# Kernel optimization log

Measured on AMD Instinct MI355X. Metric: run time of the kernel, lower is better.

## Reference

```python
import jax, jax.numpy as jnp
import numpy as np

B, S, D_MODEL, H, DK, DV, DOUT = 8, 2048, 1024, 1, 512, 512, 1024
EPS = 1e-6
TEMP = DK ** 0.5


def _ln(x, g, b):
    # LayerNorm over last dim, eps=1e-6, affine
    m = jnp.mean(x, axis=-1, keepdims=True)
    v = jnp.mean((x - m) ** 2, axis=-1, keepdims=True)
    return (x - m) * jax.lax.rsqrt(v + EPS) * g + b


def setup_inputs() -> dict:
    key = jax.random.key(0)
    ks = jax.random.split(key, 16)
    s = 0.02
    return {
        "q": jax.random.normal(ks[0], (B, S, D_MODEL), jnp.float32),
        "k": jax.random.normal(ks[1], (B, S, D_MODEL), jnp.float32),
        "v": jax.random.normal(ks[2], (B, S, D_MODEL), jnp.float32),
        "mask": jnp.ones((B, S, S), jnp.int32),
        "Wq": jax.random.normal(ks[3], (D_MODEL, H * DK), jnp.float32) * s,
        "bq": jnp.zeros((H * DK,), jnp.float32),
        "Wk": jax.random.normal(ks[4], (D_MODEL, H * DK), jnp.float32) * s,
        "bk": jnp.zeros((H * DK,), jnp.float32),
        "Wv": jax.random.normal(ks[5], (D_MODEL, H * DV), jnp.float32) * s,
        "bv": jnp.zeros((H * DV,), jnp.float32),
        "g_q": jnp.ones((H * DK,), jnp.float32),
        "be_q": jnp.zeros((H * DK,), jnp.float32),
        "g_k": jnp.ones((H * DK,), jnp.float32),
        "be_k": jnp.zeros((H * DK,), jnp.float32),
        "g_v": jnp.ones((H * DV,), jnp.float32),
        "be_v": jnp.zeros((H * DV,), jnp.float32),
        "W1": jax.random.normal(ks[6], (H * DV, H * DV), jnp.float32) * s,
        "b1": jnp.zeros((H * DV,), jnp.float32),
        "W2": jax.random.normal(ks[7], (H * DV, DOUT), jnp.float32) * s,
        "b2": jnp.zeros((DOUT,), jnp.float32),
    }


def reference(q, k, v, mask, Wq, bq, Wk, bk, Wv, bv, g_q, be_q, g_k, be_k, g_v, be_v, W1, b1, W2, b2):
    # QKV projections, viewed as (B, S, H, d)
    qp = (q @ Wq + bq).reshape(B, S, H, DK)
    kp = (k @ Wk + bk).reshape(B, S, H, DK)
    vp = (v @ Wv + bv).reshape(B, S, H, DV)
    residual = qp
    # per-(token,head) LayerNorm over last dim (valid only because H == 1 in source)
    qn = jnp.swapaxes(_ln(qp, g_q, be_q), 1, 2)  # (B, H, S, DK)
    kn = jnp.swapaxes(_ln(kp, g_k, be_k), 1, 2)
    vn = jnp.swapaxes(_ln(vp, g_v, be_v), 1, 2)
    # scaled dot-product attention with mask
    scores = jnp.einsum('bhqd,bhkd->bhqk', qn / TEMP, kn)
    scores = jnp.where(mask[:, None, :, :] == 0, -1e9, scores)
    attn = jax.nn.softmax(scores, axis=-1)
    out = jnp.einsum('bhqk,bhkd->bhqd', attn, vn)
    out = jnp.swapaxes(out, 1, 2).reshape(B, S, H * DV)
    # trailing 2-layer MLP
    out = jax.nn.relu(out @ W1 + b1) @ W2 + b2
    return (out, residual, jnp.squeeze(attn))
```

## Files before the change

### kernel.cpp

```cpp
#include <hip/hip_runtime.h>
#include <hip/hip_bf16.h>

typedef __attribute__((ext_vector_type(8))) short short8;
typedef __attribute__((ext_vector_type(4))) short short4v;
typedef __attribute__((ext_vector_type(4))) float f32x4;

#define INV_TEMP 0.044194173824159216f

__device__ __forceinline__ ushort f2bf(float f) {
  unsigned u = __float_as_uint(f);
  unsigned r = (u + 0x7FFFu + ((u >> 16) & 1u)) >> 16;
  return (ushort)r;
}
__device__ __forceinline__ float bf2f(ushort u) {
  union { unsigned i; float f; } x; x.i = ((unsigned)u) << 16; return x.f;
}

__device__ __forceinline__ void gload_lds16(const void* g, void* l) {
  __builtin_amdgcn_global_load_lds(
      (const __attribute__((address_space(1))) unsigned int*)(unsigned long long)(uintptr_t)g,
      (__attribute__((address_space(3))) unsigned int*)(unsigned)(uintptr_t)l,
      16, 0, 0);
}

__global__ __launch_bounds__(256)
void transpose_cvt_all(const float* __restrict__ Wq, const float* __restrict__ Wk,
                       const float* __restrict__ Wv, const float* __restrict__ W1,
                       const float* __restrict__ W2,
                       ushort* __restrict__ Tq, ushort* __restrict__ Tk,
                       ushort* __restrict__ Tv, ushort* __restrict__ T1,
                       ushort* __restrict__ T2) {
  const int z = blockIdx.z;
  const int K = (z < 3) ? 1024 : 512;
  const int N = (z == 4) ? 1024 : 512;
  if (blockIdx.x * 32 >= N || blockIdx.y * 32 >= K) return;
  const float* W = z == 0 ? Wq : (z == 1 ? Wk : (z == 2 ? Wv : (z == 3 ? W1 : W2)));
  ushort* WT = z == 0 ? Tq : (z == 1 ? Tk : (z == 2 ? Tv : (z == 3 ? T1 : T2)));
  __shared__ float tile[32][33];
  const int n0 = blockIdx.x * 32, k0 = blockIdx.y * 32;
  const int tx = threadIdx.x & 31, ty = threadIdx.x >> 5;
  #pragma unroll
  for (int i = ty; i < 32; i += 8)
    tile[i][tx] = W[(long)(k0 + i) * N + n0 + tx];
  __syncthreads();
  #pragma unroll
  for (int i = ty; i < 32; i += 8)
    WT[(long)(n0 + i) * K + k0 + tx] = f2bf(tile[tx][i]);
}

__global__ __launch_bounds__(256)
void transpose_bf16(const ushort* __restrict__ in, ushort* __restrict__ out, int S, int D) {
  __shared__ ushort tile[32][33];
  const ushort* inb = in + (long)blockIdx.z * S * D;
  ushort* outb = out + (long)blockIdx.z * S * D;
  const int d0 = blockIdx.x * 32, s0 = blockIdx.y * 32;
  const int tx = threadIdx.x & 31, ty = threadIdx.x >> 5;
  #pragma unroll
  for (int i = ty; i < 32; i += 8)
    tile[i][tx] = inb[(long)(s0 + i) * D + d0 + tx];
  __syncthreads();
  #pragma unroll
  for (int i = ty; i < 32; i += 8)
    outb[(long)(d0 + i) * S + s0 + tx] = tile[tx][i];
}

__global__ __launch_bounds__(256)
void ln3_kernel(const float* __restrict__ Xq, const ushort* __restrict__ Xk,
                const ushort* __restrict__ Xv,
                const float* __restrict__ gq, const float* __restrict__ beq,
                const float* __restrict__ gk, const float* __restrict__ bek,
                const float* __restrict__ gv, const float* __restrict__ bev,
                ushort* __restrict__ Oq, ushort* __restrict__ Ok, ushort* __restrict__ Ov) {
  const int which = blockIdx.y;
  const float* g = which == 0 ? gq : (which == 1 ? gk : gv);
  const float* be = which == 0 ? beq : (which == 1 ? bek : bev);
  ushort* out = which == 0 ? Oq : (which == 1 ? Ok : Ov);
  const float scale = which == 0 ? INV_TEMP : 1.0f;

  const int row = blockIdx.x * 4 + (threadIdx.x >> 6);
  const int lane = threadIdx.x & 63;
  f32x4 v0, v1;
  if (which == 0) {
    const float* x = Xq + (long)row * 512 + lane * 8;
    v0 = *(const f32x4*)x;
    v1 = *(const f32x4*)(x + 4);
  } else {
    const ushort* x = (which == 1 ? Xk : Xv) + (long)row * 512 + lane * 8;
    short8 vv = *(const short8*)x;
    #pragma unroll
    for (int j = 0; j < 4; j++) { v0[j] = bf2f((ushort)vv[j]); v1[j] = bf2f((ushort)vv[4 + j]); }
  }
  float s = v0[0]+v0[1]+v0[2]+v0[3]+v1[0]+v1[1]+v1[2]+v1[3];
  float ss = v0[0]*v0[0]+v0[1]*v0[1]+v0[2]*v0[2]+v0[3]*v0[3]
           + v1[0]*v1[0]+v1[1]*v1[1]+v1[2]*v1[2]+v1[3]*v1[3];
  #pragma unroll
  for (int off = 32; off; off >>= 1) { s += __shfl_xor(s, off); ss += __shfl_xor(ss, off); }
  const float mean = s * (1.0f/512.0f);
  const float var  = ss * (1.0f/512.0f) - mean*mean;
  const float rs = rsqrtf(var + 1e-6f);
  f32x4 g0 = *(const f32x4*)(g + lane*8);
  f32x4 g1 = *(const f32x4*)(g + lane*8 + 4);
  f32x4 b0 = *(const f32x4*)(be + lane*8);
  f32x4 b1 = *(const f32x4*)(be + lane*8 + 4);
  union { short8 v; ushort u[8]; } o;
  #pragma unroll
  for (int j = 0; j < 4; j++) o.u[j]     = f2bf(((v0[j]-mean)*rs*g0[j] + b0[j]) * scale);
  #pragma unroll
  for (int j = 0; j < 4; j++) o.u[4 + j] = f2bf(((v1[j]-mean)*rs*g1[j] + b1[j]) * scale);
  *(short8*)(out + (long)row * 512 + lane * 8) = o.v;
}

template<int EPI, bool HAS_BIAS, bool OUT_BF16, bool A_F32>
__global__ __launch_bounds__(256)
void gemm_tn_pipe(const void* __restrict__ Av, const ushort* __restrict__ Bt,
                  const float* __restrict__ bias, const int* __restrict__ mask,
                  float* __restrict__ Cf, ushort* __restrict__ Cb,
                  float* __restrict__ partial,
                  const float* __restrict__ A2, const float* __restrict__ A3,
                  const ushort* __restrict__ Bt2, const ushort* __restrict__ Bt3,
                  const float* __restrict__ bias2, const float* __restrict__ bias3,
                  ushort* __restrict__ Cb2,
                  int M, int N, int K,
                  long sA, long sB, long sC, long sMask) {
  __shared__ ushort As[2][128 * 64];
  __shared__ ushort Bs[2][128 * 64];
  __shared__ float zloc[128];
  const int tid = threadIdx.x;
  const int lane = tid & 63;
  const int wave = tid >> 6;
  const int wr = wave >> 1;
  const int wc = wave & 1;

  const int gx = gridDim.x, gy = gridDim.y;
  int lin = blockIdx.x + gx * (blockIdx.y + gy * blockIdx.z);
  const int nwg = gx * gy * (int)gridDim.z;
  int swz = lin;
  if ((nwg & 7) == 0) {
    const int q8 = nwg >> 3;
    swz = (lin & 7) * q8 + (lin >> 3);
  }
  const int bx = swz % gx;
  const int tmp = swz / gx;
  const int by = tmp % gy;
  const int bz = tmp / gy;

  const long zb = bz;
  const float* Afp;
  const ushort* Bb;
  const float* bias_p = bias;
  if constexpr (EPI == 4) {
    Afp = (bz == 0 ? (const float*)Av : (bz == 1 ? A2 : A3)) + (long)by * 128 * K;
    Bb = (bz == 0 ? Bt : (bz == 1 ? Bt2 : Bt3)) + (long)bx * 128 * K;
    bias_p = bz == 0 ? bias : (bz == 1 ? bias2 : bias3);
  } else {
    Afp = (const float*)Av + zb * sA + (long)by * 128 * K;
    Bb = Bt + zb * sB + (long)bx * 128 * K;
  }
  const ushort* Ab = (const ushort*)Av + zb * sA + (long)by * 128 * K;
  const int rowbase0 = by * 128;
  const int nt = K >> 6;

  if constexpr (EPI == 3) {
    if (tid < 128) {
      float z = 0.f;
      #pragma unroll
      for (int j = 0; j < 16; j++)
        z += partial[((long)(zb * 16 + j)) * 2048 + rowbase0 + tid];
      zloc[tid] = 1.0f / z;
    }
  }

  auto stage = [&](int buf, int t) {
    const long kt = (long)t << 6;
    if constexpr (A_F32) {
      f32x4 a[4][2];
      #pragma unroll
      for (int i = 0; i < 4; i++) {
        const int c = i * 256 + tid;
        const int row = c >> 3, g = c & 7;
        const float* p = Afp + (long)row * K + kt + g * 8;
        a[i][0] = *(const f32x4*)p;
        a[i][1] = *(const f32x4*)(p + 4);
      }
      #pragma unroll
      for (int i = 0; i < 4; i++) {
        const int c = i * 256 + tid;
        const int row = c >> 3, g = c & 7, gsrc = g ^ (row & 7);
        gload_lds16(Bb + (long)row * K + kt + gsrc * 8, (char*)Bs[buf] + c * 16);
      }
      #pragma unroll
      for (int i = 0; i < 4; i++) {
        const int c = i * 256 + tid;
        const int row = c >> 3, g = c & 7;
        union { short8 s; ushort u[8]; } o;
        #pragma unroll
        for (int j = 0; j < 4; j++) { o.u[j] = f2bf(a[i][0][j]); o.u[4 + j] = f2bf(a[i][1][j]); }
        *(short8*)((char*)As[buf] + ((row << 7) | ((g << 4) ^ ((row & 7) << 4)))) = o.s;
      }
      asm volatile("s_waitcnt lgkmcnt(0)" ::: "memory");
    } else {
      #pragma unroll
      for (int i = 0; i < 4; i++) {
        const int c = i * 256 + tid;
        const int row = c >> 3, g = c & 7, gsrc = g ^ (row & 7);
        gload_lds16(Ab + (long)row * K + kt + gsrc * 8, (char*)As[buf] + c * 16);
        gload_lds16(Bb + (long)row * K + kt + gsrc * 8, (char*)Bs[buf] + c * 16);
      }
    }
  };

  f32x4 acc[4][4];
  #pragma unroll
  for (int m = 0; m < 4; m++)
    #pragma unroll
    for (int n = 0; n < 4; n++)
      acc[m][n] = f32x4{0.f, 0.f, 0.f, 0.f};

  stage(0, 0);
  stage(1, 1);

  for (int t = 0; t < nt; ++t) {
    const int buf = t & 1;
    if (t == nt - 1) {
      asm volatile("s_waitcnt vmcnt(0)" ::: "memory");
    } else if constexpr (A_F32) {
      asm volatile("s_waitcnt vmcnt(4)" ::: "memory");
    } else {
      asm volatile("s_waitcnt vmcnt(8)" ::: "memory");
    }
    __builtin_amdgcn_s_barrier();
    __builtin_amdgcn_sched_barrier(0);

    if constexpr (EPI == 3) {
      if ((t >> 3) == bx) {
        #pragma unroll
        for (int e = 0; e < 4; e++) {
          const int c = e * 256 + tid;
          const int row = c >> 3, g = c & 7;
          short8 p8 = *(const short8*)((const char*)As[buf] +
                       ((row << 7) | ((g ^ (row & 7)) << 4)));
          const float iz = zloc[row];
          f32x4 o0, o1;
          #pragma unroll
          for (int jj = 0; jj < 4; jj++) {
            o0[jj] = bf2f((ushort)p8[jj]) * iz;
            o1[jj] = bf2f((ushort)p8[4 + jj]) * iz;
          }
          float* dst = Cf + zb * 4194304L + (long)(rowbase0 + row) * 2048 + (t << 6) + g * 8;
          *(f32x4*)dst = o0;
          *(f32x4*)(dst + 4) = o1;
        }
      }
    }

    #pragma unroll
    for (int ks = 0; ks < 2; ks++) {
      short8 af[4], bfr[4];
      const int kb = ks * 64 + ((lane >> 4) << 4);
      #pragma unroll
      for (int m = 0; m < 4; m++) {
        const int row = wr * 64 + m * 16 + (lane & 15);
        af[m] = *(const short8*)((const char*)As[buf] +
                 ((row << 7) | (kb ^ ((row & 7) << 4))));
      }
      #pragma unroll
      for (int n = 0; n < 4; n++) {
        const int col = wc * 64 + n * 16 + (lane & 15);
        bfr[n] = *(const short8*)((const char*)Bs[buf] +
                  ((col << 7) | (kb ^ ((col & 7) << 4))));
      }
      #pragma unroll
      for (int m = 0; m < 4; m++)
        #pragma unroll
        for (int n = 0; n < 4; n++)
          acc[m][n] = __builtin_amdgcn_mfma_f32_16x16x32_bf16(af[m], bfr[n], acc[m][n], 0, 0, 0);
    }
    __builtin_amdgcn_sched_barrier(0);
    __builtin_amdgcn_s_barrier();
    __builtin_amdgcn_sched_barrier(0);
    if (t + 2 < nt) stage(buf, t + 2);
  }

  const int colbase = bx * 128 + wc * 64;
  const int rowbase = by * 128 + wr * 64;
  const int c_lane = lane & 15;
  const int r_lane = (lane >> 4) << 2;

  float rs_acc[4][4];
  if constexpr (EPI == 2) {
    #pragma unroll
    for (int m = 0; m < 4; m++)
      #pragma unroll
      for (int r4 = 0; r4 < 4; r4++) rs_acc[m][r4] = 0.f;
  }

  #pragma unroll
  for (int n = 0; n < 4; n++) {
    const int col = colbase + n * 16 + c_lane;
    const float bv = HAS_BIAS ? bias_p[col] : 0.0f;
    #pragma unroll
    for (int m = 0; m < 4; m++) {
      const int rbase = rowbase + m * 16 + r_lane;
      #pragma unroll
      for (int r4 = 0; r4 < 4; r4++) {
        const int row = rbase + r4;
        float vv = acc[m][n][r4] + bv;
        if constexpr (EPI == 1) vv = fmaxf(vv, 0.0f);
        if constexpr (EPI == 2) {
          const int mk = mask[zb * sMask + (long)row * N + col];
          vv = mk ? __expf(vv) : 0.0f;
          rs_acc[m][r4] += vv;
        }
        if constexpr (EPI == 3) vv *= zloc[wr * 64 + m * 16 + r_lane + r4];
        const long off = zb * sC + (long)row * N + col;
        if constexpr (EPI == 4) {
          if (bz == 0) Cf[off] = vv;
          else if (bz == 1) Cb[off] = f2bf(vv);
          else Cb2[off] = f2bf(vv);
        } else if constexpr (OUT_BF16) {
          Cb[off] = f2bf(vv);
        } else {
          Cf[off] = vv;
        }
      }
    }
  }

  if constexpr (EPI == 2) {
    __syncthreads();
    float (*red)[128] = (float(*)[128])As;
    #pragma unroll
    for (int m = 0; m < 4; m++)
      #pragma unroll
      for (int r4 = 0; r4 < 4; r4++) {
        float vsum = rs_acc[m][r4];
        vsum += __shfl_xor(vsum, 1);
        vsum += __shfl_xor(vsum, 2);
        vsum += __shfl_xor(vsum, 4);
        vsum += __shfl_xor(vsum, 8);
        if (c_lane == 0) red[wc][wr * 64 + m * 16 + r_lane + r4] = vsum;
      }
    __syncthreads();
    if (tid < 128)
      partial[((long)zb * 16 + bx) * 2048 + by * 128 + tid] = red[0][tid] + red[1][tid];
  }
}

extern "C" void kernel_launch(void* const* d_in, const int* in_sizes, int n_in,
                              void* d_out, int out_size, void* d_ws, size_t ws_size,
                              hipStream_t stream) {
  const float* q    = (const float*)d_in[0];
  const float* k    = (const float*)d_in[1];
  const float* v    = (const float*)d_in[2];
  const int*   mask = (const int*)d_in[3];
  const float* Wq   = (const float*)d_in[4];
  const float* bq   = (const float*)d_in[5];
  const float* Wk   = (const float*)d_in[6];
  const float* bk   = (const float*)d_in[7];
  const float* Wv   = (const float*)d_in[8];
  const float* bv   = (const float*)d_in[9];
  const float* g_q  = (const float*)d_in[10];
  const float* be_q = (const float*)d_in[11];
  const float* g_k  = (const float*)d_in[12];
  const float* be_k = (const float*)d_in[13];
  const float* g_v  = (const float*)d_in[14];
  const float* be_v = (const float*)d_in[15];
  const float* W1   = (const float*)d_in[16];
  const float* b1   = (const float*)d_in[17];
  const float* W2   = (const float*)d_in[18];
  const float* b2   = (const float*)d_in[19];

  float* out_mlp  = (float*)d_out;
  float* out_res  = out_mlp + 16777216L;
  float* out_attn = out_res + 8388608L;

  char* w = (char*)d_ws;
  ushort* qn      = (ushort*)(w);
  ushort* kn      = (ushort*)(w + 16777216UL);
  ushort* kp_bf   = (ushort*)(w + 33554432UL);
  ushort* vp_bf   = (ushort*)(w + 50331648UL);
  ushort* attn_bf = (ushort*)(w + 33554432UL);
  ushort* vn      = (ushort*)(w + 100663296UL);
  ushort* vnT     = (ushort*)(w + 117440512UL);
  ushort* pv      = (ushort*)(w + 134217728UL);
  ushort* h       = (ushort*)(w + 150994944UL);
  ushort* wqT     = (ushort*)(w + 167772160UL);
  ushort* wkT     = (ushort*)(w + 168820736UL);
  ushort* wvT     = (ushort*)(w + 169869312UL);
  ushort* w1T     = (ushort*)(w + 170917888UL);
  ushort* w2T     = (ushort*)(w + 171442176UL);
  float*  partial = (float*)(w + 172490752UL);

  dim3 blk(256);

  transpose_cvt_all<<<dim3(32, 32, 5), blk, 0, stream>>>(
      Wq, Wk, Wv, W1, W2, wqT, wkT, wvT, w1T, w2T);

  gemm_tn_pipe<4, true, false, true><<<dim3(4, 128, 3), blk, 0, stream>>>(
      q, wqT, bq, nullptr, out_res, kp_bf, nullptr,
      k, v, wkT, wvT, bk, bv, vp_bf,
      16384, 512, 1024, 0, 0, 0, 0);

  ln3_kernel<<<dim3(4096, 3), blk, 0, stream>>>(
      out_res, kp_bf, vp_bf, g_q, be_q, g_k, be_k, g_v, be_v, qn, kn, vn);

  transpose_bf16<<<dim3(16, 64, 8), blk, 0, stream>>>(vn, vnT, 2048, 512);

  gemm_tn_pipe<2, false, true, false><<<dim3(16, 16, 8), blk, 0, stream>>>(
      qn, kn, nullptr, mask, nullptr, attn_bf, partial,
      nullptr, nullptr, nullptr, nullptr, nullptr, nullptr, nullptr,
      2048, 2048, 512,
      (long)2048 * 512, (long)2048 * 512, (long)2048 * 2048, (long)2048 * 2048);

  gemm_tn_pipe<3, false, true, false><<<dim3(4, 16, 8), blk, 0, stream>>>(
      attn_bf, vnT, nullptr, nullptr, out_attn, pv, partial,
      nullptr, nullptr, nullptr, nullptr, nullptr, nullptr, nullptr,
      2048, 512, 2048,
      (long)2048 * 2048, (long)512 * 2048, (long)2048 * 512, 0);

  gemm_tn_pipe<1, true, true, false><<<dim3(4, 128, 1), blk, 0, stream>>>(
      pv, w1T, b1, nullptr, nullptr, h, nullptr,
      nullptr, nullptr, nullptr, nullptr, nullptr, nullptr, nullptr,
      16384, 512, 512, 0, 0, 0, 0);
  gemm_tn_pipe<0, true, false, false><<<dim3(8, 128, 1), blk, 0, stream>>>(
      h, w2T, b2, nullptr, out_mlp, nullptr, nullptr,
      nullptr, nullptr, nullptr, nullptr, nullptr, nullptr, nullptr,
      16384, 1024, 512, 0, 0, 0, 0);
}
```

Measured before the change: 370.0 us.

## Restructure GEMM to 512 threads, K=32 tiles, triple-buffered LDS pipeline

The shared GEMM kernel now runs 8 waves per 128x128 block (2x4 wave grid, each wave owning 64x32) instead of 4 waves. It uses K-step 32 with a three-stage LDS ring instead of K-step 64 double-buffered. Prefetch for tile t+2 is issued before compute, and for f32 A operands the global load is held in registers and written to LDS after the barrier. MFMA sections are wrapped in s_setprio. The aim is more latency hiding and occupancy, at the cost of twice as many barriers per K and less MFMA work per wave between syncs.

```diff
diff --git a/kernel.cpp b/kernel.cpp
--- a/kernel.cpp
+++ b/kernel.cpp
@@ -111,7 +111,7 @@
 }
 
 template<int EPI, bool HAS_BIAS, bool OUT_BF16, bool A_F32>
-__global__ __launch_bounds__(256)
+__global__ __launch_bounds__(512, 4)
 void gemm_tn_pipe(const void* __restrict__ Av, const ushort* __restrict__ Bt,
                   const float* __restrict__ bias, const int* __restrict__ mask,
                   float* __restrict__ Cf, ushort* __restrict__ Cb,
@@ -122,14 +122,14 @@
                   ushort* __restrict__ Cb2,
                   int M, int N, int K,
                   long sA, long sB, long sC, long sMask) {
-  __shared__ ushort As[2][128 * 64];
-  __shared__ ushort Bs[2][128 * 64];
+  __shared__ ushort As[3][128 * 32];
+  __shared__ ushort Bs[3][128 * 32];
   __shared__ float zloc[128];
   const int tid = threadIdx.x;
   const int lane = tid & 63;
   const int wave = tid >> 6;
-  const int wr = wave >> 1;
-  const int wc = wave & 1;
+  const int wr = wave >> 2;
+  const int wc = wave & 3;
 
   const int gx = gridDim.x, gy = gridDim.y;
   int lin = blockIdx.x + gx * (blockIdx.y + gy * blockIdx.z);
@@ -158,7 +158,7 @@
   }
   const ushort* Ab = (const ushort*)Av + zb * sA + (long)by * 128 * K;
   const int rowbase0 = by * 128;
-  const int nt = K >> 6;
+  const int nt = K >> 5;
 
   if constexpr (EPI == 3) {
     if (tid < 128) {
@@ -170,118 +170,122 @@
     }
   }
 
-  auto stage = [&](int buf, int t) {
-    const long kt = (long)t << 6;
-    if constexpr (A_F32) {
-      f32x4 a[4][2];
-      #pragma unroll
-      for (int i = 0; i < 4; i++) {
-        const int c = i * 256 + tid;
-        const int row = c >> 3, g = c & 7;
-        const float* p = Afp + (long)row * K + kt + g * 8;
-        a[i][0] = *(const f32x4*)p;
-        a[i][1] = *(const f32x4*)(p + 4);
-      }
-      #pragma unroll
-      for (int i = 0; i < 4; i++) {
-        const int c = i * 256 + tid;
-        const int row = c >> 3, g = c & 7, gsrc = g ^ (row & 7);
-        gload_lds16(Bb + (long)row * K + kt + gsrc * 8, (char*)Bs[buf] + c * 16);
-      }
-      #pragma unroll
-      for (int i = 0; i < 4; i++) {
-        const int c = i * 256 + tid;
-        const int row = c >> 3, g = c & 7;
-        union { short8 s; ushort u[8]; } o;
-        #pragma unroll
-        for (int j = 0; j < 4; j++) { o.u[j] = f2bf(a[i][0][j]); o.u[4 + j] = f2bf(a[i][1][j]); }
-        *(short8*)((char*)As[buf] + ((row << 7) | ((g << 4) ^ ((row & 7) << 4)))) = o.s;
-      }
-      asm volatile("s_waitcnt lgkmcnt(0)" ::: "memory");
+  const int srow = tid >> 2;
+  const int sg   = tid & 3;
+  const int sgsrc = sg ^ (srow & 3);
+  const int sdst = tid * 16;
+  const int swrA = (srow << 6) | ((sg << 4) ^ ((srow & 3) << 4));
+
+  auto stageB = [&](int buf, int t) {
+    gload_lds16(Bb + (long)srow * K + ((long)t << 5) + sgsrc * 8, (char*)Bs[buf] + sdst);
+  };
+  auto stageA = [&](int buf, int t) {
+    gload_lds16(Ab + (long)srow * K + ((long)t << 5) + sgsrc * 8, (char*)As[buf] + sdst);
+  };
+  auto loadA = [&](int t, f32x4& a0, f32x4& a1) {
+    const float* p = Afp + (long)srow * K + ((long)t << 5) + sg * 8;
+    a0 = *(const f32x4*)p;
+    a1 = *(const f32x4*)(p + 4);
+  };
+  auto writeA = [&](int buf, const f32x4& a0, const f32x4& a1) {
+    union { short8 s; ushort u[8]; } o;
+    #pragma unroll
+    for (int j = 0; j < 4; j++) { o.u[j] = f2bf(a0[j]); o.u[4 + j] = f2bf(a1[j]); }
+    *(short8*)((char*)As[buf] + swrA) = o.s;
+    asm volatile("s_waitcnt lgkmcnt(0)" ::: "memory");
+  };
+
+  f32x4 acc[4][2];
+  #pragma unroll
+  for (int m = 0; m < 4; m++)
+    #pragma unroll
+    for (int n = 0; n < 2; n++)
+      acc[m][n] = f32x4{0.f, 0.f, 0.f, 0.f};
+
+  if constexpr (A_F32) {
+    f32x4 p0, p1;
+    loadA(0, p0, p1); writeA(0, p0, p1); stageB(0, 0);
+    loadA(1, p0, p1); writeA(1, p0, p1); stageB(1, 1);
+  } else {
+    stageA(0, 0); stageB(0, 0);
+    stageA(1, 1); stageB(1, 1);
+  }
+
+  for (int t = 0; t < nt; ++t) {
+    const int buf = t % 3;
+    const bool has = (t + 2 < nt);
+    f32x4 na0, na1;
+    if (has) {
+      const int nbuf = (t + 2) % 3;
+      if constexpr (A_F32) {
+        loadA(t + 2, na0, na1);
+        stageB(nbuf, t + 2);
+      } else {
+        stageA(nbuf, t + 2);
+        stageB(nbuf, t + 2);
+      }
+    }
+    const int rem = nt - 1 - t;
+    if (rem == 0) {
+      asm volatile("s_waitcnt vmcnt(0)" ::: "memory");
+    } else if (rem == 1) {
+      if constexpr (A_F32) asm volatile("s_waitcnt vmcnt(1)" ::: "memory");
+      else                 asm volatile("s_waitcnt vmcnt(2)" ::: "memory");
     } else {
-      #pragma unroll
-      for (int i = 0; i < 4; i++) {
-        const int c = i * 256 + tid;
-        const int row = c >> 3, g = c & 7, gsrc = g ^ (row & 7);
-        gload_lds16(Ab + (long)row * K + kt + gsrc * 8, (char*)As[buf] + c * 16);
-        gload_lds16(Bb + (long)row * K + kt + gsrc * 8, (char*)Bs[buf] + c * 16);
-      }
-    }
-  };
-
-  f32x4 acc[4][4];
-  #pragma unroll
-  for (int m = 0; m < 4; m++)
-    #pragma unroll
-    for (int n = 0; n < 4; n++)
-      acc[m][n] = f32x4{0.f, 0.f, 0.f, 0.f};
-
-  stage(0, 0);
-  stage(1, 1);
-
-  for (int t = 0; t < nt; ++t) {
-    const int buf = t & 1;
-    if (t == nt - 1) {
-      asm volatile("s_waitcnt vmcnt(0)" ::: "memory");
-    } else if constexpr (A_F32) {
       asm volatile("s_waitcnt vmcnt(4)" ::: "memory");
-    } else {
-      asm volatile("s_waitcnt vmcnt(8)" ::: "memory");
     }
     __builtin_amdgcn_s_barrier();
     __builtin_amdgcn_sched_barrier(0);
 
     if constexpr (EPI == 3) {
-      if ((t >> 3) == bx) {
+      if ((t >> 4) == bx) {
+        short8 p8 = *(const short8*)((const char*)As[buf] +
+                     ((srow << 6) | (((sg ^ (srow & 3))) << 4)));
+        const float iz = zloc[srow];
+        f32x4 o0, o1;
         #pragma unroll
-        for (int e = 0; e < 4; e++) {
-          const int c = e * 256 + tid;
-          const int row = c >> 3, g = c & 7;
-          short8 p8 = *(const short8*)((const char*)As[buf] +
-                       ((row << 7) | ((g ^ (row & 7)) << 4)));
-          const float iz = zloc[row];
-          f32x4 o0, o1;
-          #pragma unroll
-          for (int jj = 0; jj < 4; jj++) {
-            o0[jj] = bf2f((ushort)p8[jj]) * iz;
-            o1[jj] = bf2f((ushort)p8[4 + jj]) * iz;
-          }
-          float* dst = Cf + zb * 4194304L + (long)(rowbase0 + row) * 2048 + (t << 6) + g * 8;
-          *(f32x4*)dst = o0;
-          *(f32x4*)(dst + 4) = o1;
+        for (int jj = 0; jj < 4; jj++) {
+          o0[jj] = bf2f((ushort)p8[jj]) * iz;
+          o1[jj] = bf2f((ushort)p8[4 + jj]) * iz;
         }
-      }
-    }
-
-    #pragma unroll
-    for (int ks = 0; ks < 2; ks++) {
-      short8 af[4], bfr[4];
-      const int kb = ks * 64 + ((lane >> 4) << 4);
+        float* dst = Cf + zb * 4194304L + (long)(rowbase0 + srow) * 2048 + (t << 5) + sg * 8;
+        *(f32x4*)dst = o0;
+        *(f32x4*)(dst + 4) = o1;
+      }
+    }
+
+    {
+      short8 af[4], bfr[2];
+      const int kb = (lane >> 4) << 4;
       #pragma unroll
       for (int m = 0; m < 4; m++) {
         const int row = wr * 64 + m * 16 + (lane & 15);
         af[m] = *(const short8*)((const char*)As[buf] +
-                 ((row << 7) | (kb ^ ((row & 7) << 4))));
-      }
-      #pragma unroll
-      for (int n = 0; n < 4; n++) {
-        const int col = wc * 64 + n * 16 + (lane & 15);
+                 ((row << 6) | (kb ^ ((row & 3) << 4))));
+      }
+      #pragma unroll
+      for (int n = 0; n < 2; n++) {
+        const int col = wc * 32 + n * 16 + (lane & 15);
         bfr[n] = *(const short8*)((const char*)Bs[buf] +
-                  ((col << 7) | (kb ^ ((col & 7) << 4))));
-      }
+                  ((col << 6) | (kb ^ ((col & 3) << 4))));
+      }
+      __builtin_amdgcn_s_setprio(1);
       #pragma unroll
       for (int m = 0; m < 4; m++)
         #pragma unroll
-        for (int n = 0; n < 4; n++)
+        for (int n = 0; n < 2; n++)
           acc[m][n] = __builtin_amdgcn_mfma_f32_16x16x32_bf16(af[m], bfr[n], acc[m][n], 0, 0, 0);
+      __builtin_amdgcn_s_setprio(0);
     }
     __builtin_amdgcn_sched_barrier(0);
     __builtin_amdgcn_s_barrier();
     __builtin_amdgcn_sched_barrier(0);
-    if (t + 2 < nt) stage(buf, t + 2);
-  }
-
-  const int colbase = bx * 128 + wc * 64;
+    if (has) {
+      if constexpr (A_F32) writeA((t + 2) % 3, na0, na1);
+    }
+  }
+
+  const int colbase = bx * 128 + wc * 32;
   const int rowbase = by * 128 + wr * 64;
   const int c_lane = lane & 15;
   const int r_lane = (lane >> 4) << 2;
@@ -295,7 +299,7 @@
   }
 
   #pragma unroll
-  for (int n = 0; n < 4; n++) {
+  for (int n = 0; n < 2; n++) {
     const int col = colbase + n * 16 + c_lane;
     const float bv = HAS_BIAS ? bias_p[col] : 0.0f;
     #pragma unroll
@@ -342,7 +346,8 @@
       }
     __syncthreads();
     if (tid < 128)
-      partial[((long)zb * 16 + bx) * 2048 + by * 128 + tid] = red[0][tid] + red[1][tid];
+      partial[((long)zb * 16 + bx) * 2048 + by * 128 + tid] =
+          red[0][tid] + red[1][tid] + red[2][tid] + red[3][tid];
   }
 }
 
@@ -392,11 +397,12 @@
   float*  partial = (float*)(w + 172490752UL);
 
   dim3 blk(256);
+  dim3 blk512(512);
 
   transpose_cvt_all<<<dim3(32, 32, 5), blk, 0, stream>>>(
       Wq, Wk, Wv, W1, W2, wqT, wkT, wvT, w1T, w2T);
 
-  gemm_tn_pipe<4, true, false, true><<<dim3(4, 128, 3), blk, 0, stream>>>(
+  gemm_tn_pipe<4, true, false, true><<<dim3(4, 128, 3), blk512, 0, stream>>>(
       q, wqT, bq, nullptr, out_res, kp_bf, nullptr,
       k, v, wkT, wvT, bk, bv, vp_bf,
       16384, 512, 1024, 0, 0, 0, 0);
@@ -406,23 +412,23 @@
 
   transpose_bf16<<<dim3(16, 64, 8), blk, 0, stream>>>(vn, vnT, 2048, 512);
 
-  gemm_tn_pipe<2, false, true, false><<<dim3(16, 16, 8), blk, 0, stream>>>(
+  gemm_tn_pipe<2, false, true, false><<<dim3(16, 16, 8), blk512, 0, stream>>>(
       qn, kn, nullptr, mask, nullptr, attn_bf, partial,
       nullptr, nullptr, nullptr, nullptr, nullptr, nullptr, nullptr,
       2048, 2048, 512,
       (long)2048 * 512, (long)2048 * 512, (long)2048 * 2048, (long)2048 * 2048);
 
-  gemm_tn_pipe<3, false, true, false><<<dim3(4, 16, 8), blk, 0, stream>>>(
+  gemm_tn_pipe<3, false, true, false><<<dim3(4, 16, 8), blk512, 0, stream>>>(
       attn_bf, vnT, nullptr, nullptr, out_attn, pv, partial,
       nullptr, nullptr, nullptr, nullptr, nullptr, nullptr, nullptr,
       2048, 512, 2048,
       (long)2048 * 2048, (long)512 * 2048, (long)2048 * 512, 0);
 
-  gemm_tn_pipe<1, true, true, false><<<dim3(4, 128, 1), blk, 0, stream>>>(
+  gemm_tn_pipe<1, true, true, false><<<dim3(4, 128, 1), blk512, 0, stream>>>(
       pv, w1T, b1, nullptr, nullptr, h, nullptr,
       nullptr, nullptr, nullptr, nullptr, nullptr, nullptr, nullptr,
       16384, 512, 512, 0, 0, 0, 0);
-  gemm_tn_pipe<0, true, false, false><<<dim3(8, 128, 1), blk, 0, stream>>>(
+  gemm_tn_pipe<0, true, false, false><<<dim3(8, 128, 1), blk512, 0, stream>>>(
       h, w2T, b2, nullptr, out_mlp, nullptr, nullptr,
       nullptr, nullptr, nullptr, nullptr, nullptr, nullptr, nullptr,
       16384, 1024, 512, 0, 0, 0, 0);
```

New measurement: 387.2 us. 1.05x slower.
